# Performance work log

Hardware: AMD Instinct MI355X
Metric: run time of the kernel (lower is better)

The kernel has to match this reference:

```python
import jax, jax.numpy as jnp
import numpy as np

B, T, C, H, NT = 1, 1024, 768, 12, 8
D = C // H  # 64
POWER_ITERS = 4
DP_TEMP = 0.8
ESR_GAMMA = 0.02
ESR_ALPHA = 0.1


def rmsnorm(x, w, eps=1e-6):
    rms = jax.lax.rsqrt(jnp.mean(x * x, axis=-1, keepdims=True) + eps)
    return x * rms * w


def setup_inputs():
    key = jax.random.key(0)
    k0, k1, k2 = jax.random.split(key, 3)
    return {
        "x": jax.random.normal(k0, (B, T, C), jnp.float32),
        "W_qkvg": jax.random.normal(k1, (4 * C, C), jnp.float32) * 0.02,
        "W_out": jax.random.normal(k2, (C, C), jnp.float32) * 0.02,
        "lam": jnp.float32(1.5),
        "log_tau": -0.5 * jnp.ones((H, NT), jnp.float32),
        "logit_w": jnp.zeros((H, NT), jnp.float32),
        "beta": 1.5 * jnp.ones((H,), jnp.float32),
        "out_scale": jnp.ones((H,), jnp.float32),
        "dp_scale": jnp.ones((H,), jnp.float32),
        "logk_scale": jnp.ones((H,), jnp.float32),
        "dt_logit": jnp.float32(np.log(1.0 / 1e-8)),  # dt=1.0 -> logit = log(dt/(1-dt+1e-8))
        "g_norm_w": jnp.ones((D,), jnp.float32),
    }


def reference(x, W_qkvg, W_out, lam, log_tau, logit_w, beta, out_scale,
              dp_scale, logk_scale, dt_logit, g_norm_w):
    # qkvg projection and head split
    qkvg = x @ W_qkvg.T                                    # [B,T,4C]
    q, k, v, g = jnp.split(qkvg, 4, axis=-1)
    to_heads = lambda t: t.reshape(B, T, H, D).transpose(0, 2, 1, 3)  # [B,H,T,D]
    q, k, v, g = map(to_heads, (q, k, v, g))
    g = rmsnorm(g, g_norm_w)

    # pairwise squared distance ||g_i - g_j||^2
    g2 = jnp.sum(g * g, axis=-1)                           # [B,H,T]
    s = jnp.maximum(g2[..., :, None] + g2[..., None, :]
                    - 2.0 * jnp.einsum('bhid,bhjd->bhij', g, g), 0.0)  # [B,H,T,T]

    # fractional log-kernel: logsumexp_t[-(beta/2) log1p(s/(4 tau_t)) + log w_t]
    tau = jnp.maximum(jnp.exp(log_tau), 1e-6)              # [H,NT]
    w = jax.nn.softmax(logit_w, axis=-1)                   # [H,NT]
    beta_c = jnp.clip(beta, 0.5, 2.5)                      # [H]
    log_k_per = -(beta_c[None, :, None, None, None] / 2.0) * jnp.log1p(
        s[:, :, None] / (4.0 * tau[None, :, :, None, None]))          # [B,H,NT,T,T]
    logK = jax.nn.logsumexp(log_k_per + jnp.log(w + 1e-12)[None, :, :, None, None], axis=2)
    logK = logK * logk_scale[None, :, None, None]

    # dot-product scores
    dp = jnp.einsum('bhid,bhjd->bhij', q, k) * (dp_scale[None, :, None, None]
                                                / (np.sqrt(D) * DP_TEMP))

    # causal Markov normalize: blend, mask, stable row-softmax
    mask = jnp.tril(jnp.ones((T, T), bool))[None, None]    # [1,1,T,T]
    blended = lam * dp + (1.0 - lam) * logK
    blended = jnp.where(mask, blended, -jnp.inf)
    mx = jnp.max(blended, axis=-1, keepdims=True)
    mx = jnp.where(jnp.isfinite(mx), mx, 0.0)
    Kmat = jnp.exp(jnp.maximum(blended - mx, -60.0)) * mask
    P = Kmat / jnp.maximum(Kmat.sum(-1, keepdims=True), 1e-12)

    # power iteration for left stationary pi with full-support teleport
    pi0 = jnp.full((B, H, 1, T), 1.0 / T, P.dtype)
    def step(pi, _):
        p = (1.0 - ESR_GAMMA) * (pi @ P) + ESR_GAMMA / T
        p = p / jnp.maximum(p.sum(-1, keepdims=True), 1e-12)
        return p, None
    pi, _ = jax.lax.scan(step, pi0, None, length=POWER_ITERS)
    pi = jax.lax.stop_gradient(pi[..., 0, :])              # [B,H,T] (detached)

    # causal approximation to additive reversibilization
    P_adj = (pi[..., None, :] / jnp.maximum(pi[..., :, None], 1e-12)) \
            * jnp.swapaxes(P, -1, -2)                      # P*_ij = (pi_j/pi_i) P_ji
    P_rev = 0.5 * (P + P_adj) * mask
    P_rev = P_rev / jnp.maximum(P_rev.sum(-1, keepdims=True), 1e-12)

    dt = jax.nn.sigmoid(dt_logit)
    alpha = ESR_ALPHA * dt                                  # scale_alpha_by_dt=True
    P_fin = (1.0 - alpha) * P + alpha * P_rev

    y = (P_fin @ v) * out_scale[None, :, None, None]       # [B,H,T,D]
    y = y.transpose(0, 2, 1, 3).reshape(B, T, C)
    return y @ W_out.T
```

## Files before the change

kernel.cpp:

```cpp
#include <hip/hip_runtime.h>
#include <math.h>

#define TSEQ 1024
#define CD   768
#define HN   12
#define DD   64
#define CH   4

#define OFF_QH     0
#define OFF_KH     393216
#define OFF_GH     786432
#define OFF_VHT    1179648
#define OFF_VH     1572864
#define OFF_G2     1966080
#define OFF_YB     1978368
#define OFF_CONSTS 2371584
#define OFF_OPART  2372096
#define OFF_LS     5517824
#define OFF_PD     5566976
#define OFF_XB     5579264
#define OFF_WQB    5972480
#define OFF_WOB    7152128

#define NG_X  98304
#define NG_WQ 294912
#define NG_WO 73728

typedef __bf16 bf16x8 __attribute__((ext_vector_type(8)));
typedef float  f32x4  __attribute__((ext_vector_type(4)));
typedef unsigned short u16x8 __attribute__((ext_vector_type(8)));
typedef unsigned short u16x4 __attribute__((ext_vector_type(4)));

__device__ inline unsigned short f2bf(float f) {
  unsigned int u = __float_as_uint(f);
  return (unsigned short)((u + 0x7fffu + ((u >> 16) & 1u)) >> 16);
}
__device__ inline float bf2f(unsigned short u) {
  return __uint_as_float((unsigned)u << 16);
}


__global__ __launch_bounds__(256) void convert_kernel(
    const float* __restrict__ x, const float* __restrict__ wq,
    const float* __restrict__ wo, unsigned short* __restrict__ swzA,
    unsigned short* __restrict__ swzWQ, unsigned short* __restrict__ swzWO,
    const float* __restrict__ lam_p, const float* __restrict__ log_tau,
    const float* __restrict__ logit_w, const float* __restrict__ beta,
    const float* __restrict__ out_scale, const float* __restrict__ dp_scale,
    const float* __restrict__ logk_scale, const float* __restrict__ dt_logit,
    float* __restrict__ consts) {
  if (blockIdx.x == 0 && threadIdx.x < 64) {
    int h = threadIdx.x;
    if (h == 0) {
      float dt = 1.0f / (1.0f + __expf(-dt_logit[0]));
      consts[288] = 0.1f * dt;
    }
    if (h < HN) {
      float lam = lam_p[0];
      float* c = consts + h * 24;
      c[0] = lam * dp_scale[h] * (1.0f / 6.4f);
      c[1] = (1.0f - lam) * logk_scale[h];
      float b = fminf(fmaxf(beta[h], 0.5f), 2.5f);
      c[2] = 0.5f * b;
      c[3] = out_scale[h];
      float m = -1e30f;
      float lw[8];
      bool uni = true;
      for (int t = 0; t < 8; t++) {
        lw[t] = logit_w[h * 8 + t];
        m = fmaxf(m, lw[t]);
        if (log_tau[h * 8 + t] != log_tau[h * 8] || lw[t] != lw[0]) uni = false;
      }
      float s = 0.f;
      float e[8];
      for (int t = 0; t < 8; t++) { e[t] = __expf(lw[t] - m); s += e[t]; }
      for (int t = 0; t < 8; t++) {
        float w = e[t] / s;
        c[12 + t] = log2f(w + 1e-12f);
        float tau = fmaxf(__expf(log_tau[h * 8 + t]), 1e-6f);
        c[4 + t] = 1.0f / (4.0f * tau);
      }
      c[20] = uni ? 1.0f : 8.0f;
    }
  }
  int g = blockIdx.x * 256 + threadIdx.x;
  const float* src;
  unsigned short* dst;
  int lg;
  if (g < NG_X) { src = x; dst = swzA; lg = g; }
  else if (g < NG_X + NG_WQ) { src = wq; dst = swzWQ; lg = g - NG_X; }
  else if (g < NG_X + NG_WQ + NG_WO) { src = wo; dst = swzWO; lg = g - NG_X - NG_WQ; }
  else return;
  int lane = lg & 63;
  int kb = (lg >> 6) % 24;
  int t16 = lg / (64 * 24);
  int row = t16 * 16 + (lane & 15);
  int col = kb * 32 + (lane >> 4) * 8;
  const float* s = &src[(size_t)row * 768 + col];
  float4 a = *(const float4*)s;
  float4 b = *(const float4*)(s + 4);
  u16x8 u;
  u[0] = f2bf(a.x); u[1] = f2bf(a.y); u[2] = f2bf(a.z); u[3] = f2bf(a.w);
  u[4] = f2bf(b.x); u[5] = f2bf(b.y); u[6] = f2bf(b.z); u[7] = f2bf(b.w);
  *(u16x8*)&dst[(size_t)lg * 8] = u;
}

__global__ __launch_bounds__(256) void gemm_frag_qkvg(
    const unsigned short* __restrict__ swzA, const unsigned short* __restrict__ swzB,
    const float* __restrict__ consts, const float* __restrict__ g_norm_w,
    unsigned short* __restrict__ qh, unsigned short* __restrict__ kh,
    unsigned short* __restrict__ gh, unsigned short* __restrict__ vh,
    unsigned short* __restrict__ vhT, float* __restrict__ g2) {
  __shared__ __align__(16) unsigned short Ls[128 * 72];
  int t = threadIdx.x, lane = t & 63, w = t >> 6;
  int quad = lane >> 4, tx = lane & 15;
  int ntile = blockIdx.x;
  int m0 = blockIdx.y * 128;
  int nt0 = ntile * 4;
  int mt0 = blockIdx.y * 8 + w * 2;

  f32x4 acc[2][4] = {};
#pragma unroll 2
  for (int kb = 0; kb < 24; kb++) {
    bf16x8 a0 = *(const bf16x8*)&swzA[((size_t)((mt0 + 0) * 24 + kb) * 64 + lane) * 8];
    bf16x8 a1 = *(const bf16x8*)&swzA[((size_t)((mt0 + 1) * 24 + kb) * 64 + lane) * 8];
#pragma unroll
    for (int ni = 0; ni < 4; ni++) {
      bf16x8 b = *(const bf16x8*)&swzB[((size_t)((nt0 + ni) * 24 + kb) * 64 + lane) * 8];
      acc[0][ni] = __builtin_amdgcn_mfma_f32_16x16x32_bf16(a0, b, acc[0][ni], 0, 0, 0);
      acc[1][ni] = __builtin_amdgcn_mfma_f32_16x16x32_bf16(a1, b, acc[1][ni], 0, 0, 0);
    }
  }

  int typ = ntile / 12;
  int h = ntile % 12;
  unsigned short* Lw = Ls + w * (32 * 72);
  int mrow0 = m0 + w * 32;

  if (typ == 3) {
    float gw4[4];
#pragma unroll
    for (int ni = 0; ni < 4; ni++) gw4[ni] = g_norm_w[ni * 16 + tx];
#pragma unroll
    for (int mi = 0; mi < 2; mi++) {
#pragma unroll
      for (int reg = 0; reg < 4; reg++) {
        float s1 = acc[mi][0][reg] * acc[mi][0][reg] + acc[mi][1][reg] * acc[mi][1][reg]
                 + acc[mi][2][reg] * acc[mi][2][reg] + acc[mi][3][reg] * acc[mi][3][reg];
#pragma unroll
        for (int m = 1; m < 16; m <<= 1) s1 += __shfl_xor(s1, m, 64);
        float rms = rsqrtf(s1 * (1.f / 64.f) + 1e-6f);
        int rl = mi * 16 + quad * 4 + reg;
        float s2 = 0.f;
#pragma unroll
        for (int ni = 0; ni < 4; ni++) {
          float v = acc[mi][ni][reg] * rms * gw4[ni];
          unsigned short us = f2bf(v);
          Lw[rl * 72 + ni * 16 + tx] = us;
          float vb = bf2f(us);
          s2 += vb * vb;
        }
#pragma unroll
        for (int m = 1; m < 16; m <<= 1) s2 += __shfl_xor(s2, m, 64);
        if (tx == 0) g2[h * 1024 + mrow0 + rl] = s2;
      }
    }
#pragma unroll
    for (int rep = 0; rep < 4; rep++) {
      int idx = rep * 64 + lane;
      int r = idx >> 3, cc = (idx & 7) * 8;
      *(u16x8*)&gh[(size_t)(h * 1024 + mrow0 + r) * 64 + cc] = *(const u16x8*)&Lw[r * 72 + cc];
    }
  } else {
    float sc = (typ == 0) ? consts[h * 24] * 1.44269504089f : 1.0f;
#pragma unroll
    for (int mi = 0; mi < 2; mi++)
#pragma unroll
      for (int ni = 0; ni < 4; ni++)
#pragma unroll
        for (int reg = 0; reg < 4; reg++) {
          int rl = mi * 16 + quad * 4 + reg;
          Lw[rl * 72 + ni * 16 + tx] = f2bf(acc[mi][ni][reg] * sc);
        }
    unsigned short* dst = (typ == 0) ? qh : ((typ == 1) ? kh : vh);
#pragma unroll
    for (int rep = 0; rep < 4; rep++) {
      int idx = rep * 64 + lane;
      int r = idx >> 3, cc = (idx & 7) * 8;
      *(u16x8*)&dst[(size_t)(h * 1024 + mrow0 + r) * 64 + cc] = *(const u16x8*)&Lw[r * 72 + cc];
    }
    if (typ == 2) {
#pragma unroll
      for (int rep = 0; rep < 4; rep++) {
        int idx = rep * 64 + lane;
        int d = idx >> 2, rc = (idx & 3) * 8;
        u16x8 u;
#pragma unroll
        for (int j = 0; j < 8; j++) u[j] = Lw[(rc + j) * 72 + d];
        *(u16x8*)&vhT[(size_t)(h * 64 + d) * 1024 + mrow0 + rc] = u;
      }
    }
  }
}

__global__ __launch_bounds__(256) void gemm_frag_out(
    const unsigned short* __restrict__ swzA, const unsigned short* __restrict__ swzB,
    float* __restrict__ Cm) {
  int t = threadIdx.x, lane = t & 63, w = t >> 6;
  int quad = lane >> 4, tx = lane & 15;
  int n0 = blockIdx.x * 64;
  int m0 = blockIdx.y * 128;
  int nt0 = blockIdx.x * 4;
  int mt0 = blockIdx.y * 8 + w * 2;

  f32x4 acc[2][4] = {};
#pragma unroll 2
  for (int kb = 0; kb < 24; kb++) {
    bf16x8 a0 = *(const bf16x8*)&swzA[((size_t)((mt0 + 0) * 24 + kb) * 64 + lane) * 8];
    bf16x8 a1 = *(const bf16x8*)&swzA[((size_t)((mt0 + 1) * 24 + kb) * 64 + lane) * 8];
#pragma unroll
    for (int ni = 0; ni < 4; ni++) {
      bf16x8 b = *(const bf16x8*)&swzB[((size_t)((nt0 + ni) * 24 + kb) * 64 + lane) * 8];
      acc[0][ni] = __builtin_amdgcn_mfma_f32_16x16x32_bf16(a0, b, acc[0][ni], 0, 0, 0);
      acc[1][ni] = __builtin_amdgcn_mfma_f32_16x16x32_bf16(a1, b, acc[1][ni], 0, 0, 0);
    }
  }
#pragma unroll
  for (int mi = 0; mi < 2; mi++)
#pragma unroll
    for (int ni = 0; ni < 4; ni++)
#pragma unroll
      for (int reg = 0; reg < 4; reg++) {
        int row = m0 + w * 32 + mi * 16 + quad * 4 + reg;
        Cm[(size_t)row * CD + n0 + ni * 16 + tx] = acc[mi][ni][reg];
      }
}

__global__ __launch_bounds__(256, 4) void flash_kernel(
    const unsigned short* __restrict__ qh, const unsigned short* __restrict__ kh,
    const unsigned short* __restrict__ gh, const unsigned short* __restrict__ vhT,
    const float* __restrict__ g2, const float* __restrict__ consts,
    float* __restrict__ Opart, float* __restrict__ lsp, float* __restrict__ pdp) {
  int h = blockIdx.y;
  int uu = 79 - (int)blockIdx.x;
  int it = 0, rem = uu;
  for (it = 0; it < 32; ++it) {
    int njt_ = (it >> 1) + 1;
    int nc = (njt_ + CH - 1) / CH;
    if (rem < nc) break;
    rem -= nc;
  }
  int njt = (it >> 1) + 1;
  int jt0 = rem * CH;
  int jt1 = (jt0 + CH < njt) ? (jt0 + CH) : njt;
  bool owns_diag = (jt1 == njt);
  int i0 = it * 32;
  int t = threadIdx.x;
  int lane = t & 63, w = t >> 6;
  int quad = lane >> 4, tx = lane & 15;
  int mi = w >> 1, nb = (w & 1) * 2;

  __shared__ __align__(16) unsigned short Ks[64 * 72];
  __shared__ __align__(16) unsigned short Gjs[64 * 72];
  __shared__ __align__(16) unsigned short Vt[64 * 72];
  __shared__ __align__(16) unsigned short psh[32 * 72];
  __shared__ float g2i[32], g2j[64], pdiag[32], lsum[32];

  const float* ch = consts + h * 24;
  float lkc = ch[1], bh2 = ch[2];
  int ntt = (int)ch[20];
  float i4t0 = ch[4];
  float inv4tau[8], logw[8];
#pragma unroll
  for (int tt = 0; tt < 8; tt++) { inv4tau[tt] = ch[4 + tt]; logw[tt] = ch[12 + tt]; }

  {
    int r = t >> 3, c8 = (t & 7) * 8;
    *(u16x8*)&Ks[r * 72 + c8] = *(const u16x8*)&qh[(size_t)(h * 1024 + i0 + r) * 64 + c8];
    *(u16x8*)&Gjs[r * 72 + c8] = *(const u16x8*)&gh[(size_t)(h * 1024 + i0 + r) * 64 + c8];
  }
  if (t < 32) { g2i[t] = g2[h * 1024 + i0 + t]; pdiag[t] = 0.f; }
  __syncthreads();

  bf16x8 aq[2], ag[2];
#pragma unroll
  for (int ks = 0; ks < 2; ks++) {
    aq[ks] = *(const bf16x8*)&Ks[(mi * 16 + tx) * 72 + ks * 32 + quad * 8];
    ag[ks] = *(const bf16x8*)&Gjs[(mi * 16 + tx) * 72 + ks * 32 + quad * 8];
  }

  f32x4 Oc[2] = {};
  float rowacc[4] = {0.f, 0.f, 0.f, 0.f};
  int r4 = t >> 2, cb = (t & 3) * 16;

  u16x8 pk0, pk1, pg0, pg1, pv0, pv1;
  float pg2 = 0.f;
  {
    int j0 = jt0 * 64;
    const unsigned short* kp = &kh[(size_t)(h * 1024 + j0 + r4) * 64 + cb];
    const unsigned short* gp = &gh[(size_t)(h * 1024 + j0 + r4) * 64 + cb];
    const unsigned short* vp = &vhT[(size_t)(h * 64 + r4) * 1024 + j0 + cb];
    pk0 = *(const u16x8*)kp; pk1 = *(const u16x8*)(kp + 8);
    pg0 = *(const u16x8*)gp; pg1 = *(const u16x8*)(gp + 8);
    pv0 = *(const u16x8*)vp; pv1 = *(const u16x8*)(vp + 8);
    if (t < 64) pg2 = g2[h * 1024 + j0 + t];
  }

  for (int jt = jt0; jt < jt1; jt++) {
    int j0 = jt * 64;
    __syncthreads();
    *(u16x8*)&Ks[r4 * 72 + cb] = pk0;
    *(u16x8*)&Ks[r4 * 72 + cb + 8] = pk1;
    *(u16x8*)&Gjs[r4 * 72 + cb] = pg0;
    *(u16x8*)&Gjs[r4 * 72 + cb + 8] = pg1;
    *(u16x8*)&Vt[r4 * 72 + cb] = pv0;
    *(u16x8*)&Vt[r4 * 72 + cb + 8] = pv1;
    if (t < 64) g2j[t] = pg2;
    __syncthreads();

    if (jt + 1 < jt1) {
      int jn = j0 + 64;
      const unsigned short* kp = &kh[(size_t)(h * 1024 + jn + r4) * 64 + cb];
      const unsigned short* gp = &gh[(size_t)(h * 1024 + jn + r4) * 64 + cb];
      const unsigned short* vp = &vhT[(size_t)(h * 64 + r4) * 1024 + jn + cb];
      pk0 = *(const u16x8*)kp; pk1 = *(const u16x8*)(kp + 8);
      pg0 = *(const u16x8*)gp; pg1 = *(const u16x8*)(gp + 8);
      pv0 = *(const u16x8*)vp; pv1 = *(const u16x8*)(vp + 8);
      if (t < 64) pg2 = g2[h * 1024 + jn + t];
    }

    f32x4 sqk[2] = {}, sgg[2] = {};
#pragma unroll
    for (int ni2 = 0; ni2 < 2; ni2++) {
#pragma unroll
      for (int ks = 0; ks < 2; ks++) {
        bf16x8 bk = *(const bf16x8*)&Ks[((nb + ni2) * 16 + tx) * 72 + ks * 32 + quad * 8];
        sqk[ni2] = __builtin_amdgcn_mfma_f32_16x16x32_bf16(aq[ks], bk, sqk[ni2], 0, 0, 0);
        bf16x8 bg = *(const bf16x8*)&Gjs[((nb + ni2) * 16 + tx) * 72 + ks * 32 + quad * 8];
        sgg[ni2] = __builtin_amdgcn_mfma_f32_16x16x32_bf16(ag[ks], bg, sgg[ni2], 0, 0, 0);
      }
    }

    float rs[4] = {0.f, 0.f, 0.f, 0.f};
#pragma unroll
    for (int ni2 = 0; ni2 < 2; ni2++) {
      int colg = j0 + (nb + ni2) * 16 + tx;
      float g2jv = g2j[(nb + ni2) * 16 + tx];
#pragma unroll
      for (int reg = 0; reg < 4; reg++) {
        int rowl = mi * 16 + quad * 4 + reg;
        int gi = i0 + rowl;
        float s = fmaxf(g2i[rowl] + g2jv - 2.0f * sgg[ni2][reg], 0.0f);
        float lse2;
        if (ntt == 1) {
          lse2 = -bh2 * __builtin_amdgcn_logf(fmaf(s, i4t0, 1.0f));
        } else {
          float se = 0.f;
#pragma unroll
          for (int tt = 0; tt < 8; tt++) {
            float lv = __builtin_amdgcn_logf(fmaf(s, inv4tau[tt], 1.0f));
            se += __builtin_amdgcn_exp2f(fmaf(-bh2, lv, logw[tt]));
          }
          lse2 = __builtin_amdgcn_logf(se + 1e-30f);
        }
        float b = fmaf(lkc, lse2, sqk[ni2][reg]);
        float p = (colg <= gi) ? __builtin_amdgcn_exp2f(b) : 0.0f;
        rs[reg] += p;
        psh[rowl * 72 + (nb + ni2) * 16 + tx] = f2bf(p);
        if (colg == gi) pdiag[rowl] = p;
      }
    }
#pragma unroll
    for (int reg = 0; reg < 4; reg++) {
#pragma unroll
      for (int m = 1; m < 16; m <<= 1) rs[reg] += __shfl_xor(rs[reg], m, 64);
      rowacc[reg] += rs[reg];
    }
    __syncthreads();

    bf16x8 ap[2];
#pragma unroll
    for (int ks = 0; ks < 2; ks++)
      ap[ks] = *(const bf16x8*)&psh[(mi * 16 + tx) * 72 + ks * 32 + quad * 8];
#pragma unroll
    for (int nd2 = 0; nd2 < 2; nd2++) {
#pragma unroll
      for (int ks = 0; ks < 2; ks++) {
        bf16x8 bv = *(const bf16x8*)&Vt[((nb + nd2) * 16 + tx) * 72 + ks * 32 + quad * 8];
        Oc[nd2] = __builtin_amdgcn_mfma_f32_16x16x32_bf16(ap[ks], bv, Oc[nd2], 0, 0, 0);
      }
    }
  }

  if ((w & 1) == 0 && tx == 0) {
#pragma unroll
    for (int reg = 0; reg < 4; reg++) lsum[mi * 16 + quad * 4 + reg] = rowacc[reg];
  }
  __syncthreads();
  if ((w & 1) == 1 && tx == 0) {
#pragma unroll
    for (int reg = 0; reg < 4; reg++) {
      int rowl = mi * 16 + quad * 4 + reg;
      lsp[(size_t)(rem * HN + h) * 1024 + i0 + rowl] = lsum[rowl] + rowacc[reg];
    }
  }
  float* Ob = Opart + (size_t)((rem * HN + h) * 1024 + i0) * 64;
#pragma unroll
  for (int nd2 = 0; nd2 < 2; nd2++) {
#pragma unroll
    for (int reg = 0; reg < 4; reg++) {
      int rowl = mi * 16 + quad * 4 + reg;
      Ob[rowl * 64 + (nb + nd2) * 16 + tx] = Oc[nd2][reg];
    }
  }
  if (owns_diag && t < 32) pdp[h * 1024 + i0 + t] = pdiag[t];
}

__global__ __launch_bounds__(256) void finalize_kernel(
    const float* __restrict__ Opart, const float* __restrict__ lsp,
    const float* __restrict__ pdp, const unsigned short* __restrict__ vh,
    const float* __restrict__ consts, unsigned short* __restrict__ yb) {
  int h = blockIdx.y;
  int t = threadIdx.x;
  int rl = t >> 4, d4 = t & 15;
  int gi = blockIdx.x * 16 + rl;
  int it = gi >> 5;
  int njt = (it >> 1) + 1;
  int nc = (njt + CH - 1) / CH;
  float alpha = consts[288];
  float osc = consts[h * 24 + 3];
  float4 Ov = make_float4(0.f, 0.f, 0.f, 0.f);
  float l = 0.f;
  for (int c = 0; c < nc; c++) {
    float4 p = *(const float4*)&Opart[(size_t)((c * HN + h) * 1024 + gi) * 64 + 4 * d4];
    Ov.x += p.x; Ov.y += p.y; Ov.z += p.z; Ov.w += p.w;
    l += lsp[(size_t)(c * HN + h) * 1024 + gi];
  }
  l = fmaxf(l, 1e-12f);
  float Pii = pdp[h * TSEQ + gi] / l;
  float inv1p = 1.0f / (1.0f + Pii);
  float c1 = (1.0f - alpha) + alpha * inv1p;
  float c2 = alpha * Pii * inv1p;
  float invl = 1.0f / l;
  u16x4 vb = *(const u16x4*)&vh[(size_t)(h * 1024 + gi) * 64 + 4 * d4];
  u16x4 o;
  o[0] = f2bf(osc * (c1 * Ov.x * invl + c2 * bf2f(vb[0])));
  o[1] = f2bf(osc * (c1 * Ov.y * invl + c2 * bf2f(vb[1])));
  o[2] = f2bf(osc * (c1 * Ov.z * invl + c2 * bf2f(vb[2])));
  o[3] = f2bf(osc * (c1 * Ov.w * invl + c2 * bf2f(vb[3])));
  int k = h * 64 + 4 * d4;
  int kb = k >> 5, q8 = (k & 31) >> 3, j0 = k & 7;
  int mt = gi >> 4, txl = gi & 15;
  size_t off = (((size_t)mt * 24 + kb) * 64 + q8 * 16 + txl) * 8 + j0;
  *(u16x4*)&yb[off] = o;
}

extern "C" void kernel_launch(void* const* d_in, const int* in_sizes, int n_in,
                              void* d_out, int out_size, void* d_ws, size_t ws_size,
                              hipStream_t stream) {
  (void)in_sizes; (void)n_in; (void)out_size; (void)ws_size;
  const float* x          = (const float*)d_in[0];
  const float* W_qkvg     = (const float*)d_in[1];
  const float* W_out      = (const float*)d_in[2];
  const float* lam        = (const float*)d_in[3];
  const float* log_tau    = (const float*)d_in[4];
  const float* logit_w    = (const float*)d_in[5];
  const float* beta       = (const float*)d_in[6];
  const float* out_scale  = (const float*)d_in[7];
  const float* dp_scale   = (const float*)d_in[8];
  const float* logk_scale = (const float*)d_in[9];
  const float* dt_logit   = (const float*)d_in[10];
  const float* g_norm_w   = (const float*)d_in[11];
  float* ws = (float*)d_ws;
  unsigned short* qh  = (unsigned short*)(ws + OFF_QH);
  unsigned short* kh  = (unsigned short*)(ws + OFF_KH);
  unsigned short* gh  = (unsigned short*)(ws + OFF_GH);
  unsigned short* vhT = (unsigned short*)(ws + OFF_VHT);
  unsigned short* vh  = (unsigned short*)(ws + OFF_VH);
  float* g2     = ws + OFF_G2;
  unsigned short* yb  = (unsigned short*)(ws + OFF_YB);
  float* consts = ws + OFF_CONSTS;
  float* Opart  = ws + OFF_OPART;
  float* lsp    = ws + OFF_LS;
  float* pdp    = ws + OFF_PD;
  unsigned short* swzA = (unsigned short*)(ws + OFF_XB);
  unsigned short* swzWQ = (unsigned short*)(ws + OFF_WQB);
  unsigned short* swzWO = (unsigned short*)(ws + OFF_WOB);
  float* out = (float*)d_out;

  convert_kernel<<<dim3((NG_X + NG_WQ + NG_WO) / 256), dim3(256), 0, stream>>>(
      x, W_qkvg, W_out, swzA, swzWQ, swzWO,
      lam, log_tau, logit_w, beta, out_scale, dp_scale, logk_scale, dt_logit, consts);
  gemm_frag_qkvg<<<dim3(48, 8), dim3(256), 0, stream>>>(swzA, swzWQ, consts, g_norm_w,
                                                        qh, kh, gh, vh, vhT, g2);
  flash_kernel<<<dim3(80, 12), dim3(256), 0, stream>>>(qh, kh, gh, vhT, g2, consts,
                                                       Opart, lsp, pdp);
  finalize_kernel<<<dim3(64, 12), dim3(256), 0, stream>>>(Opart, lsp, pdp, vh, consts, yb);
  gemm_frag_out<<<dim3(12, 8), dim3(256), 0, stream>>>(yb, swzWO, out);
}
```

Baseline: 151.2 us.

## Compute row sums via MFMA with ones vector, mask only diagonal tile, add setprio

```diff
diff --git a/kernel.cpp b/kernel.cpp
--- a/kernel.cpp
+++ b/kernel.cpp
@@ -264,7 +264,7 @@
   __shared__ __align__(16) unsigned short Gjs[64 * 72];
   __shared__ __align__(16) unsigned short Vt[64 * 72];
   __shared__ __align__(16) unsigned short psh[32 * 72];
-  __shared__ float g2i[32], g2j[64], pdiag[32], lsum[32];
+  __shared__ float g2i[32], g2j[64], pdiag[32];
 
   const float* ch = consts + h * 24;
   float lkc = ch[1], bh2 = ch[2];
@@ -274,23 +274,6 @@
 #pragma unroll
   for (int tt = 0; tt < 8; tt++) { inv4tau[tt] = ch[4 + tt]; logw[tt] = ch[12 + tt]; }
 
-  {
-    int r = t >> 3, c8 = (t & 7) * 8;
-    *(u16x8*)&Ks[r * 72 + c8] = *(const u16x8*)&qh[(size_t)(h * 1024 + i0 + r) * 64 + c8];
-    *(u16x8*)&Gjs[r * 72 + c8] = *(const u16x8*)&gh[(size_t)(h * 1024 + i0 + r) * 64 + c8];
-  }
-  if (t < 32) { g2i[t] = g2[h * 1024 + i0 + t]; pdiag[t] = 0.f; }
-  __syncthreads();
-
-  bf16x8 aq[2], ag[2];
-#pragma unroll
-  for (int ks = 0; ks < 2; ks++) {
-    aq[ks] = *(const bf16x8*)&Ks[(mi * 16 + tx) * 72 + ks * 32 + quad * 8];
-    ag[ks] = *(const bf16x8*)&Gjs[(mi * 16 + tx) * 72 + ks * 32 + quad * 8];
-  }
-
-  f32x4 Oc[2] = {};
-  float rowacc[4] = {0.f, 0.f, 0.f, 0.f};
   int r4 = t >> 2, cb = (t & 3) * 16;
 
   u16x8 pk0, pk1, pg0, pg1, pv0, pv1;
@@ -306,8 +289,30 @@
     if (t < 64) pg2 = g2[h * 1024 + j0 + t];
   }
 
+  {
+    int r = t >> 3, c8 = (t & 7) * 8;
+    *(u16x8*)&Ks[r * 72 + c8] = *(const u16x8*)&qh[(size_t)(h * 1024 + i0 + r) * 64 + c8];
+    *(u16x8*)&Gjs[r * 72 + c8] = *(const u16x8*)&gh[(size_t)(h * 1024 + i0 + r) * 64 + c8];
+  }
+  if (t < 32) { g2i[t] = g2[h * 1024 + i0 + t]; pdiag[t] = 0.f; }
+  __syncthreads();
+
+  bf16x8 aq[2], ag[2];
+#pragma unroll
+  for (int ks = 0; ks < 2; ks++) {
+    aq[ks] = *(const bf16x8*)&Ks[(mi * 16 + tx) * 72 + ks * 32 + quad * 8];
+    ag[ks] = *(const bf16x8*)&Gjs[(mi * 16 + tx) * 72 + ks * 32 + quad * 8];
+  }
+
+  __bf16 onebf = (__bf16)((tx == 0) ? 1.0f : 0.0f);
+  bf16x8 bones = {onebf, onebf, onebf, onebf, onebf, onebf, onebf, onebf};
+
+  f32x4 Oc[2] = {};
+  f32x4 Osum = {};
+
   for (int jt = jt0; jt < jt1; jt++) {
     int j0 = jt * 64;
+    bool masked = (jt == njt - 1);
     __syncthreads();
     *(u16x8*)&Ks[r4 * 72 + cb] = pk0;
     *(u16x8*)&Ks[r4 * 72 + cb + 8] = pk1;
@@ -330,6 +335,7 @@
     }
 
     f32x4 sqk[2] = {}, sgg[2] = {};
+    __builtin_amdgcn_s_setprio(1);
 #pragma unroll
     for (int ni2 = 0; ni2 < 2; ni2++) {
 #pragma unroll
@@ -340,16 +346,14 @@
         sgg[ni2] = __builtin_amdgcn_mfma_f32_16x16x32_bf16(ag[ks], bg, sgg[ni2], 0, 0, 0);
       }
     }
-
-    float rs[4] = {0.f, 0.f, 0.f, 0.f};
+    __builtin_amdgcn_s_setprio(0);
+
 #pragma unroll
     for (int ni2 = 0; ni2 < 2; ni2++) {
-      int colg = j0 + (nb + ni2) * 16 + tx;
       float g2jv = g2j[(nb + ni2) * 16 + tx];
 #pragma unroll
       for (int reg = 0; reg < 4; reg++) {
         int rowl = mi * 16 + quad * 4 + reg;
-        int gi = i0 + rowl;
         float s = fmaxf(g2i[rowl] + g2jv - 2.0f * sgg[ni2][reg], 0.0f);
         float lse2;
         if (ntt == 1) {
@@ -364,17 +368,15 @@
           lse2 = __builtin_amdgcn_logf(se + 1e-30f);
         }
         float b = fmaf(lkc, lse2, sqk[ni2][reg]);
-        float p = (colg <= gi) ? __builtin_amdgcn_exp2f(b) : 0.0f;
-        rs[reg] += p;
+        float p = __builtin_amdgcn_exp2f(b);
+        if (masked) {
+          int colg = j0 + (nb + ni2) * 16 + tx;
+          int gi = i0 + rowl;
+          if (colg > gi) p = 0.0f;
+          if (colg == gi) pdiag[rowl] = p;
+        }
         psh[rowl * 72 + (nb + ni2) * 16 + tx] = f2bf(p);
-        if (colg == gi) pdiag[rowl] = p;
-      }
-    }
-#pragma unroll
-    for (int reg = 0; reg < 4; reg++) {
-#pragma unroll
-      for (int m = 1; m < 16; m <<= 1) rs[reg] += __shfl_xor(rs[reg], m, 64);
-      rowacc[reg] += rs[reg];
+      }
     }
     __syncthreads();
 
@@ -382,6 +384,7 @@
 #pragma unroll
     for (int ks = 0; ks < 2; ks++)
       ap[ks] = *(const bf16x8*)&psh[(mi * 16 + tx) * 72 + ks * 32 + quad * 8];
+    __builtin_amdgcn_s_setprio(1);
 #pragma unroll
     for (int nd2 = 0; nd2 < 2; nd2++) {
 #pragma unroll
@@ -390,19 +393,18 @@
         Oc[nd2] = __builtin_amdgcn_mfma_f32_16x16x32_bf16(ap[ks], bv, Oc[nd2], 0, 0, 0);
       }
     }
+    if ((w & 1) == 0) {
+#pragma unroll
+      for (int ks = 0; ks < 2; ks++)
+        Osum = __builtin_amdgcn_mfma_f32_16x16x32_bf16(ap[ks], bones, Osum, 0, 0, 0);
+    }
+    __builtin_amdgcn_s_setprio(0);
   }
 
   if ((w & 1) == 0 && tx == 0) {
 #pragma unroll
-    for (int reg = 0; reg < 4; reg++) lsum[mi * 16 + quad * 4 + reg] = rowacc[reg];
-  }
-  __syncthreads();
-  if ((w & 1) == 1 && tx == 0) {
-#pragma unroll
-    for (int reg = 0; reg < 4; reg++) {
-      int rowl = mi * 16 + quad * 4 + reg;
-      lsp[(size_t)(rem * HN + h) * 1024 + i0 + rowl] = lsum[rowl] + rowacc[reg];
-    }
+    for (int reg = 0; reg < 4; reg++)
+      lsp[(size_t)(rem * HN + h) * 1024 + i0 + mi * 16 + quad * 4 + reg] = Osum[reg];
   }
   float* Ob = Opart + (size_t)((rem * HN + h) * 1024 + i0) * 64;
 #pragma unroll
```

Result: faster. 146.4 us (-3.2%).
